# Kernel tuning notes

Measured on AMD Instinct MI355X. Metric: run time of the kernel, lower is better.

## Reference

```python
import jax, jax.numpy as jnp
import numpy as np

B, T, S, D = 8, 512, 512, 1024
NUM_HEADS = 16
REUSE_HEADS = 8
NEW_HEADS = NUM_HEADS - REUSE_HEADS
KEY_DIM = 64
VALUE_DIM = 64
PE_MAX = 512  # pe_max_seq_length


def setup_inputs() -> dict:
    key = jax.random.key(0)
    ks = jax.random.split(key, 12)
    s = 0.02
    return {
        "query": jax.random.normal(ks[0], (B, T, D), jnp.float32),
        "value": jax.random.normal(ks[1], (B, S, D), jnp.float32),
        # scores reused from a previous layer (already softmaxed there)
        "reuse_attention_scores": jax.random.uniform(ks[2], (B, REUSE_HEADS, T, S), jnp.float32),
        "Wq": jax.random.normal(ks[3], (D, NEW_HEADS, KEY_DIM), jnp.float32) * s,
        "bq": jnp.zeros((NEW_HEADS, KEY_DIM), jnp.float32),
        "Wk": jax.random.normal(ks[4], (D, NEW_HEADS, KEY_DIM), jnp.float32) * s,
        "bk": jnp.zeros((NEW_HEADS, KEY_DIM), jnp.float32),
        "Wv": jax.random.normal(ks[5], (D, NUM_HEADS, VALUE_DIM), jnp.float32) * s,
        "bv": jnp.zeros((NUM_HEADS, VALUE_DIM), jnp.float32),
        # relative position embeddings: [1, new_heads, 2*PE_MAX - 1]
        "pos_emb": jax.random.truncated_normal(ks[6], -2.0, 2.0, (1, NEW_HEADS, 2 * PE_MAX - 1), jnp.float32) * 0.2,
        # output denses: one for reused heads (no bias), one for new heads (bias)
        "Wo_reuse": jax.random.normal(ks[7], (REUSE_HEADS, VALUE_DIM, D), jnp.float32) * s,
        "Wo_new": jax.random.normal(ks[8], (NEW_HEADS, VALUE_DIM, D), jnp.float32) * s,
        "bo": jnp.zeros((D,), jnp.float32),
    }


def reference(query, value, reuse_attention_scores, Wq, bq, Wk, bk, Wv, bv,
              pos_emb, Wo_reuse, Wo_new, bo):
    # projections (EinsumDense abc,cde->abde + bias over last two dims)
    q = jnp.einsum("btd,dnh->btnh", query, Wq) + bq           # [B,T,Hn,kd]
    k = jnp.einsum("bsd,dnh->bsnh", value, Wk) + bk           # [B,S,Hn,kd]
    v = jnp.einsum("bsd,dnh->bsnh", value, Wv) + bv           # [B,S,H,vd]
    v_reuse, v_new = v[:, :, :REUSE_HEADS, :], v[:, :, REUSE_HEADS:, :]

    # new-head scores: scaled QK^T  (dot_product_equation 'aecd,abcd->acbe')
    q = q * (1.0 / np.sqrt(float(KEY_DIM)))
    new_scores = jnp.einsum("bsnh,btnh->bnts", k, q)          # [B,Hn,T,S]

    # relative position bias: index = clip(key_pos - query_pos + PE_MAX-1)
    rel = jnp.arange(S)[None, :] - jnp.arange(T)[:, None] + (PE_MAX - 1)
    rel = jnp.clip(rel, 0, 2 * PE_MAX - 2)                    # [T,S]
    bias = pos_emb[0][:, rel]                                 # [Hn,T,S]
    new_scores = jax.nn.softmax(new_scores + bias[None], axis=-1)

    # reused heads consume previous-layer scores directly (dropout=0)
    reuse_scores = reuse_attention_scores[:, :REUSE_HEADS]
    out_reuse = jnp.einsum("bnts,bsnh->btnh", reuse_scores, v_reuse)
    out_new = jnp.einsum("bnts,bsnh->btnh", new_scores, v_new)

    # separate output projections, summed; bias only on the new-heads dense
    out = (jnp.einsum("btnh,nhd->btd", out_reuse, Wo_reuse)
           + jnp.einsum("btnh,nhd->btd", out_new, Wo_new) + bo)
    return out
```

## Files before the change

kernel.cpp:

```cpp
#include <hip/hip_runtime.h>
#include <hip/hip_bf16.h>

typedef __bf16 bf16_t;
typedef __bf16 bf16x8 __attribute__((ext_vector_type(8)));
typedef __bf16 bf16x4v __attribute__((ext_vector_type(4)));
typedef float  f32x4  __attribute__((ext_vector_type(4)));

#define GLDS(gsrc, ldst)                                                              \
  __builtin_amdgcn_global_load_lds(                                                   \
      (const __attribute__((address_space(1))) unsigned int*)(gsrc),                  \
      (__attribute__((address_space(3))) unsigned int*)(ldst), 16, 0, 0)

struct TArgs {
  const float* src[5];
  bf16_t* dst[5];
  int C[5], Ct[5], off[5], blk0[6];
  float scale[5];
};
struct CTArgs {
  const float* qa; bf16_t* qd;
  const float* va; bf16_t* vd;
  TArgs ta;
};
__global__ void k_convtrans(CTArgs ca) {
  __shared__ float tile[32][33];
  const int bid = blockIdx.x;
  if (bid < 4096) {
    int i = bid * 256 + threadIdx.x;
    const float* s; bf16_t* d;
    if (i < 524288) { s = ca.qa; d = ca.qd; } else { s = ca.va; d = ca.vd; i -= 524288; }
    const float4* p = reinterpret_cast<const float4*>(s) + 2 * (long)i;
    float4 x = p[0], y = p[1];
    bf16x8 o;
    o[0] = (bf16_t)x.x; o[1] = (bf16_t)x.y; o[2] = (bf16_t)x.z; o[3] = (bf16_t)x.w;
    o[4] = (bf16_t)y.x; o[5] = (bf16_t)y.y; o[6] = (bf16_t)y.z; o[7] = (bf16_t)y.w;
    reinterpret_cast<bf16x8*>(d)[i] = o;
    return;
  }
  const TArgs& ta = ca.ta;
  const int tb = bid - 4096;
  int s = 0;
  while (tb >= ta.blk0[s + 1]) ++s;
  const int bi = tb - ta.blk0[s];
  const int Ct = ta.Ct[s];
  const int c0 = (bi % Ct) * 32, r0 = (bi / Ct) * 32;
  const int C = ta.C[s];
  const float* src = ta.src[s];
  const int lx = threadIdx.x & 31, ly = threadIdx.x >> 5;
  #pragma unroll
  for (int i = 0; i < 32; i += 8)
    tile[ly + i][lx] = src[(long)(r0 + ly + i) * C + (c0 + lx)];
  __syncthreads();
  const float sc = ta.scale[s];
  bf16_t* dst = ta.dst[s];
  const int off = ta.off[s];
  #pragma unroll
  for (int i = 0; i < 32; i += 8)
    dst[(long)(c0 + ly + i) * 1024 + off + (r0 + lx)] = (bf16_t)(tile[lx][ly + i] * sc);
}

struct ProjItem {
  const bf16_t* A; const bf16_t* B; bf16_t* C; const float* bias;
  float bscale; int ldc; int writeT;
};
struct ProjArgs { ProjItem it[3]; };

__global__ __launch_bounds__(256)
void k_gemm_proj(ProjArgs pa) {
  __shared__ char smem[32768];
  const int bid = blockIdx.x;
  const int z = bid < 128 ? 0 : (bid < 256 ? 1 : 2);
  const int local = bid - (z == 0 ? 0 : (z == 1 ? 128 : 256));
  const ProjItem it = pa.it[z];
  const int t = threadIdx.x, lane = t & 63, wid = t >> 6;
  const int wr = wid >> 1, wc = wid & 1;
  const int m0 = (local & 31) * 128, n0 = (local >> 5) * 128;
  const int lhi = lane >> 4, llo = lane & 15;

  const bf16_t* Ab = it.A + (long)m0 * 1024;
  const bf16_t* Bb = it.B + (long)n0 * 1024;

  const int e0 = t * 8,        r0s = e0 >> 5, c0s = e0 & 31;
  const int e1 = (256 + t) * 8, r1s = e1 >> 5, c1s = e1 & 31;

#define PSTAGE(k0_, bsel)                                                     \
  { bf16_t* bA = (bf16_t*)(smem + (bsel) * 16384);                            \
    bf16_t* bB = (bf16_t*)(smem + (bsel) * 16384 + 8192);                     \
    GLDS(Ab + (long)r0s * 1024 + (k0_) + c0s, bA + wid * 512);                \
    GLDS(Ab + (long)r1s * 1024 + (k0_) + c1s, bA + 2048 + wid * 512);         \
    GLDS(Bb + (long)r0s * 1024 + (k0_) + c0s, bB + wid * 512);                \
    GLDS(Bb + (long)r1s * 1024 + (k0_) + c1s, bB + 2048 + wid * 512); }

  f32x4 acc[4][4] = {};
  PSTAGE(0, 0);
  __syncthreads();
  int cur = 0;
  for (int t32 = 0; t32 < 32; ++t32) {
    bf16_t* sA = (bf16_t*)(smem + cur * 16384);
    bf16_t* sB = (bf16_t*)(smem + cur * 16384 + 8192);
    bf16x8 a[4], b[4];
    #pragma unroll
    for (int mi = 0; mi < 4; ++mi)
      a[mi] = *reinterpret_cast<const bf16x8*>(sA + (wr * 64 + mi * 16 + llo) * 32 + lhi * 8);
    #pragma unroll
    for (int ni = 0; ni < 4; ++ni)
      b[ni] = *reinterpret_cast<const bf16x8*>(sB + (wc * 64 + ni * 16 + llo) * 32 + lhi * 8);
    if (t32 < 31) PSTAGE((t32 + 1) * 32, cur ^ 1);
    #pragma unroll
    for (int mi = 0; mi < 4; ++mi)
      #pragma unroll
      for (int ni = 0; ni < 4; ++ni)
        acc[mi][ni] = __builtin_amdgcn_mfma_f32_16x16x32_bf16(a[mi], b[ni], acc[mi][ni], 0, 0, 0);
    __syncthreads();
    cur ^= 1;
  }
#undef PSTAGE

  #pragma unroll
  for (int mi = 0; mi < 4; ++mi)
    #pragma unroll
    for (int ni = 0; ni < 4; ++ni) {
      const float bv = it.bias[n0 + wc * 64 + ni * 16 + llo] * it.bscale;
      #pragma unroll
      for (int r = 0; r < 4; ++r) acc[mi][ni][r] += bv;
    }

  if (!it.writeT) {
    bf16_t* E = (bf16_t*)smem;
    #pragma unroll
    for (int p = 0; p < 2; ++p) {
      if (wr == p) {
        #pragma unroll
        for (int mi = 0; mi < 4; ++mi)
          #pragma unroll
          for (int ni = 0; ni < 4; ++ni)
            #pragma unroll
            for (int r = 0; r < 4; ++r)
              E[(mi * 16 + lhi * 4 + r) * 136 + wc * 64 + ni * 16 + llo] = (bf16_t)acc[mi][ni][r];
      }
      __syncthreads();
      #pragma unroll
      for (int round = 0; round < 4; ++round) {
        const int row = (t >> 4) + round * 16;
        const int l16 = t & 15;
        float4 v = *reinterpret_cast<const float4*>((char*)E + row * 272 + l16 * 16);
        *reinterpret_cast<float4*>(it.C + (long)(m0 + p * 64 + row) * it.ldc + n0 + l16 * 8) = v;
      }
      __syncthreads();
    }
  } else {
    bf16_t* E = (bf16_t*)smem;
    #pragma unroll
    for (int p = 0; p < 2; ++p) {
      if (wr == p) {
        #pragma unroll
        for (int mi = 0; mi < 4; ++mi)
          #pragma unroll
          for (int ni = 0; ni < 4; ++ni)
            #pragma unroll
            for (int r = 0; r < 4; ++r)
              E[(wc * 64 + ni * 16 + llo) * 72 + mi * 16 + lhi * 4 + r] = (bf16_t)acc[mi][ni][r];
      }
      __syncthreads();
      #pragma unroll
      for (int round = 0; round < 4; ++round) {
        const int nr = (t >> 3) + round * 32;
        const int l8 = t & 7;
        float4 v = *reinterpret_cast<const float4*>((char*)E + nr * 144 + l8 * 16);
        *reinterpret_cast<float4*>(it.C + (long)(n0 + nr) * it.ldc + m0 + p * 64 + l8 * 8) = v;
      }
      __syncthreads();
    }
  }
}

__global__ __launch_bounds__(256)
void k_gemm_out(const bf16_t* __restrict__ A_, const bf16_t* __restrict__ B_,
                float* __restrict__ C_, const float* __restrict__ bias) {
  __shared__ char smem[24576];
  const int t = threadIdx.x, lane = t & 63, wid = t >> 6;
  const int wr = wid >> 1, wc = wid & 1;
  const int m0 = blockIdx.x * 64, n0 = blockIdx.y * 128;
  const int lhi = lane >> 4, llo = lane & 15;

  const bf16_t* Ab = A_ + (long)m0 * 1024;
  const bf16_t* Bb = B_ + (long)n0 * 1024;

  const int e0 = t * 8,        r0s = e0 >> 5, c0s = e0 & 31;
  const int e1 = (256 + t) * 8, r1s = e1 >> 5, c1s = e1 & 31;

#define OSTAGE(k0_, bsel)                                                     \
  { bf16_t* bA = (bf16_t*)(smem + (bsel) * 12288);                            \
    bf16_t* bB = (bf16_t*)(smem + (bsel) * 12288 + 4096);                     \
    GLDS(Ab + (long)r0s * 1024 + (k0_) + c0s, bA + wid * 512);                \
    GLDS(Bb + (long)r0s * 1024 + (k0_) + c0s, bB + wid * 512);                \
    GLDS(Bb + (long)r1s * 1024 + (k0_) + c1s, bB + 2048 + wid * 512); }

  f32x4 acc[2][4] = {};
  OSTAGE(0, 0);
  __syncthreads();
  int cur = 0;
  for (int t32 = 0; t32 < 32; ++t32) {
    bf16_t* sA = (bf16_t*)(smem + cur * 12288);
    bf16_t* sB = (bf16_t*)(smem + cur * 12288 + 4096);
    bf16x8 a[2], b[4];
    #pragma unroll
    for (int mi = 0; mi < 2; ++mi)
      a[mi] = *reinterpret_cast<const bf16x8*>(sA + (wr * 32 + mi * 16 + llo) * 32 + lhi * 8);
    #pragma unroll
    for (int ni = 0; ni < 4; ++ni)
      b[ni] = *reinterpret_cast<const bf16x8*>(sB + (wc * 64 + ni * 16 + llo) * 32 + lhi * 8);
    if (t32 < 31) OSTAGE((t32 + 1) * 32, cur ^ 1);
    #pragma unroll
    for (int mi = 0; mi < 2; ++mi)
      #pragma unroll
      for (int ni = 0; ni < 4; ++ni)
        acc[mi][ni] = __builtin_amdgcn_mfma_f32_16x16x32_bf16(a[mi], b[ni], acc[mi][ni], 0, 0, 0);
    __syncthreads();
    cur ^= 1;
  }
#undef OSTAGE

  #pragma unroll
  for (int mi = 0; mi < 2; ++mi)
    #pragma unroll
    for (int ni = 0; ni < 4; ++ni) {
      const float bv = bias[n0 + wc * 64 + ni * 16 + llo];
      #pragma unroll
      for (int r = 0; r < 4; ++r) acc[mi][ni][r] += bv;
    }

  float* E = (float*)smem;
  #pragma unroll
  for (int p = 0; p < 2; ++p) {
    if (wr == p) {
      #pragma unroll
      for (int mi = 0; mi < 2; ++mi)
        #pragma unroll
        for (int ni = 0; ni < 4; ++ni)
          #pragma unroll
          for (int r = 0; r < 4; ++r)
            E[(mi * 16 + lhi * 4 + r) * 132 + wc * 64 + ni * 16 + llo] = acc[mi][ni][r];
    }
    __syncthreads();
    #pragma unroll
    for (int round = 0; round < 4; ++round) {
      const int row = (t >> 5) + round * 8;
      const int l32 = t & 31;
      float4 v = *reinterpret_cast<const float4*>((char*)E + row * 528 + l32 * 16);
      *reinterpret_cast<float4*>(C_ + (long)(m0 + p * 32 + row) * 1024 + n0 + l32 * 4) = v;
    }
    __syncthreads();
  }
}

__global__ __launch_bounds__(256, 5)
void k_attn_all(const bf16_t* __restrict__ qb, const bf16_t* __restrict__ kb,
                const bf16_t* __restrict__ vbT, const float* __restrict__ pe,
                const float* __restrict__ reuse, bf16_t* __restrict__ om) {
  __shared__ char smem[32768];
  const int bid = blockIdx.x;
  const int r3 = bid % 3;
  const int q3 = bid / 3;
  const int lane = threadIdx.x & 63, w = threadIdx.x >> 6;
  const int lhi = lane >> 4, llo = lane & 15;

  if (r3 == 0) {
    bf16_t* pes2 = (bf16_t*)smem;
    char* KtB = smem + 8192;
    char* VtB = smem + 16384;
    char* PtB = smem + 24576 + w * 2048;

    const int fidx = q3;
    const int tt = fidx >> 6;
    const int bh = fidx & 63;
    const int b = bh >> 3, h = bh & 7;
    const int t0w = tt * 64 + w * 16;

    const bf16_t* Ksrc = kb + (long)(b * 512) * 512 + h * 64;
    const bf16_t* Vsrc = vbT + (long)(512 + h * 64) * 4096 + b * 512;
    const int krow = w * 16 + (lane >> 3);
    const int kcol = ((lane & 7) ^ (lane >> 3)) << 3;
    bf16_t* kdst = (bf16_t*)(KtB + w * 2048);
    bf16_t* vdst = (bf16_t*)(VtB + w * 2048);

#define STAGE_K(it_)                                                                   \
  { _Pragma("unroll")                                                                  \
    for (int g = 0; g < 2; ++g)                                                        \
      GLDS(Ksrc + (long)((it_) * 64 + krow + g * 8) * 512 + kcol, kdst + g * 512); }
#define STAGE_V(it_)                                                                   \
  { _Pragma("unroll")                                                                  \
    for (int g = 0; g < 2; ++g)                                                        \
      GLDS(Vsrc + (long)(krow + g * 8) * 4096 + (it_) * 64 + kcol, vdst + g * 512); }

    STAGE_K(0);
    STAGE_V(0);

    const bf16_t* Qb = qb + (long)(b * 512 + t0w + llo) * 512 + h * 64;
    bf16x8 qf0 = *reinterpret_cast<const bf16x8*>(Qb + lhi * 8);
    bf16x8 qf1 = *reinterpret_cast<const bf16x8*>(Qb + 32 + lhi * 8);
    {
      const float* peh = pe + h * 1023;
      for (int j = threadIdx.x; j < 4092; j += 256) {
        const int d = j >> 2, st = j & 3;
        int idx = d + 16 * st; if (idx > 1022) idx = 1022;
        pes2[j] = (bf16_t)peh[idx];
      }
    }

    f32x4 oacc[4] = {};
    float lr[4] = {0.f, 0.f, 0.f, 0.f};

    __syncthreads();

    for (int it = 0; it < 8; ++it) {
      const int s0 = it * 64;

      f32x4 acc[4] = {};
      #pragma unroll
      for (int st = 0; st < 4; ++st) {
        const int rowb = st * 16 + llo;
        const int sw = (rowb & 7) << 4;
        bf16x8 kf0 = *reinterpret_cast<const bf16x8*>(KtB + rowb * 128 + ((lhi * 16) ^ sw));
        bf16x8 kf1 = *reinterpret_cast<const bf16x8*>(KtB + rowb * 128 + ((64 + lhi * 16) ^ sw));
        acc[st] = __builtin_amdgcn_mfma_f32_16x16x32_bf16(qf0, kf0, acc[st], 0, 0, 0);
        acc[st] = __builtin_amdgcn_mfma_f32_16x16x32_bf16(qf1, kf1, acc[st], 0, 0, 0);
      }

      __syncthreads();
      if (it < 7) STAGE_K(it + 1);

      #pragma unroll
      for (int r = 0; r < 4; ++r) {
        const int tl = lhi * 4 + r;
        const int bidx = s0 + llo - (t0w + tl) + 511;
        const bf16x4v pb = *reinterpret_cast<const bf16x4v*>(pes2 + bidx * 4);
        const int swp = (tl & 7) << 4;
        float lp = 0.f;
        #pragma unroll
        for (int st = 0; st < 4; ++st) {
          const float e = __expf(acc[st][r] + (float)pb[st]);
          lp += e;
          *reinterpret_cast<bf16_t*>(PtB + tl * 128 + (((st * 16 + llo) * 2) ^ swp)) = (bf16_t)e;
        }
        lr[r] += lp;
      }

      const int swa = (llo & 7) << 4;
      #pragma unroll
      for (int ks = 0; ks < 2; ++ks) {
        bf16x8 pav = *reinterpret_cast<const bf16x8*>(PtB + llo * 128 + ((ks * 64 + lhi * 16) ^ swa));
        #pragma unroll
        for (int ni = 0; ni < 4; ++ni) {
          const int rowv = ni * 16 + llo;
          bf16x8 vf = *reinterpret_cast<const bf16x8*>(VtB + rowv * 128 + ((ks * 64 + lhi * 16) ^ ((rowv & 7) << 4)));
          oacc[ni] = __builtin_amdgcn_mfma_f32_16x16x32_bf16(pav, vf, oacc[ni], 0, 0, 0);
        }
      }

      __syncthreads();
      if (it < 7) STAGE_V(it + 1);
    }

    #pragma unroll
    for (int r = 0; r < 4; ++r) {
      lr[r] += __shfl_xor(lr[r], 1);
      lr[r] += __shfl_xor(lr[r], 2);
      lr[r] += __shfl_xor(lr[r], 4);
      lr[r] += __shfl_xor(lr[r], 8);
    }

    bf16_t* Ew = (bf16_t*)(smem + 8192 + w * 4096);
    #pragma unroll
    for (int ni = 0; ni < 4; ++ni)
      #pragma unroll
      for (int r = 0; r < 4; ++r)
        Ew[(lhi * 4 + r) * 72 + ni * 16 + llo] = (bf16_t)(oacc[ni][r] * (1.f / lr[r]));
    #pragma unroll
    for (int round = 0; round < 2; ++round) {
      const int lr8 = (lane >> 3) + round * 8;
      const int l8 = lane & 7;
      float4 v = *reinterpret_cast<const float4*>((char*)Ew + lr8 * 144 + l8 * 16);
      *reinterpret_cast<float4*>(om + (long)(b * 512 + t0w + lr8) * 1024 + 512 + h * 64 + l8 * 8) = v;
    }
#undef STAGE_K
#undef STAGE_V
    return;
  }

  typedef float RedRow[32][68];
  RedRow* red = (RedRow*)smem;
  const int pidx = q3 * 2 + (r3 - 1);
  const int bh = pidx & 63;
  const int mt = pidx >> 6;
  const int b = bh >> 3, head = bh & 7;
  const int m0 = mt * 32;
  const int ks0 = w * 128;

  const float*  Af = reuse + (long)b * 2097152 + (long)head * 262144;
  const bf16_t* Bp = vbT + (long)(head * 64) * 4096 + b * 512;

  f32x4 acc[2][4] = {};
  float4 Ax[2][2][2];
  bf16x8 Bx[2][4];

  #define PV_LOAD(kq, buf)                                                              \
    {                                                                                   \
      const int kk = ks0 + (kq) * 32 + lhi * 8;                                         \
      _Pragma("unroll")                                                                 \
      for (int mi = 0; mi < 2; ++mi) {                                                  \
        const float4* p = reinterpret_cast<const float4*>(Af + (long)(m0 + mi * 16 + llo) * 512 + kk); \
        Ax[buf][mi][0] = p[0];                                                          \
        Ax[buf][mi][1] = p[1];                                                          \
      }                                                                                 \
      _Pragma("unroll")                                                                 \
      for (int ni = 0; ni < 4; ++ni)                                                    \
        Bx[buf][ni] = *reinterpret_cast<const bf16x8*>(Bp + (long)(ni * 16 + llo) * 4096 + kk); \
    }

  PV_LOAD(0, 0);
  #pragma unroll
  for (int kq = 0; kq < 4; ++kq) {
    const int cb = kq & 1;
    if (kq < 3) {
      const int nb = (kq + 1) & 1;
      PV_LOAD(kq + 1, nb);
    }
    bf16x8 a[2];
    #pragma unroll
    for (int mi = 0; mi < 2; ++mi) {
      float4 x = Ax[cb][mi][0], y = Ax[cb][mi][1];
      bf16x8 tv;
      tv[0] = (bf16_t)x.x; tv[1] = (bf16_t)x.y; tv[2] = (bf16_t)x.z; tv[3] = (bf16_t)x.w;
      tv[4] = (bf16_t)y.x; tv[5] = (bf16_t)y.y; tv[6] = (bf16_t)y.z; tv[7] = (bf16_t)y.w;
      a[mi] = tv;
    }
    #pragma unroll
    for (int mi = 0; mi < 2; ++mi)
      #pragma unroll
      for (int ni = 0; ni < 4; ++ni)
        acc[mi][ni] = __builtin_amdgcn_mfma_f32_16x16x32_bf16(a[mi], Bx[cb][ni], acc[mi][ni], 0, 0, 0);
  }
  #undef PV_LOAD

  if (w >= 2) {
    #pragma unroll
    for (int mi = 0; mi < 2; ++mi)
      #pragma unroll
      for (int ni = 0; ni < 4; ++ni)
        #pragma unroll
        for (int r = 0; r < 4; ++r)
          red[w - 2][mi * 16 + lhi * 4 + r][ni * 16 + llo] = acc[mi][ni][r];
  }
  __syncthreads();
  if (w < 2) {
    #pragma unroll
    for (int mi = 0; mi < 2; ++mi)
      #pragma unroll
      for (int ni = 0; ni < 4; ++ni)
        #pragma unroll
        for (int r = 0; r < 4; ++r)
          acc[mi][ni][r] += red[w][mi * 16 + lhi * 4 + r][ni * 16 + llo];
  }
  __syncthreads();
  if (w == 1) {
    #pragma unroll
    for (int mi = 0; mi < 2; ++mi)
      #pragma unroll
      for (int ni = 0; ni < 4; ++ni)
        #pragma unroll
        for (int r = 0; r < 4; ++r)
          red[0][mi * 16 + lhi * 4 + r][ni * 16 + llo] = acc[mi][ni][r];
  }
  __syncthreads();
  if (w == 0) {
    bf16_t* E = (bf16_t*)&red[1][0][0];
    #pragma unroll
    for (int mi = 0; mi < 2; ++mi)
      #pragma unroll
      for (int ni = 0; ni < 4; ++ni)
        #pragma unroll
        for (int r = 0; r < 4; ++r) {
          const int mr = mi * 16 + lhi * 4 + r;
          const int nn = ni * 16 + llo;
          E[mr * 72 + nn] = (bf16_t)(acc[mi][ni][r] + red[0][mr][nn]);
        }
    bf16_t* Cb = om + (long)b * 524288 + head * 64;
    #pragma unroll
    for (int round = 0; round < 4; ++round) {
      const int row = (lane >> 3) + round * 8;
      const int l8 = lane & 7;
      float4 v = *reinterpret_cast<const float4*>((char*)E + row * 144 + l8 * 16);
      *reinterpret_cast<float4*>(Cb + (long)(m0 + row) * 1024 + l8 * 8) = v;
    }
  }
}

extern "C" void kernel_launch(void* const* d_in, const int* in_sizes, int n_in,
                              void* d_out, int out_size, void* d_ws, size_t ws_size,
                              hipStream_t stream) {
  const float* query = (const float*)d_in[0];
  const float* value = (const float*)d_in[1];
  const float* reuse = (const float*)d_in[2];
  const float* Wq    = (const float*)d_in[3];
  const float* bq    = (const float*)d_in[4];
  const float* Wk    = (const float*)d_in[5];
  const float* bk    = (const float*)d_in[6];
  const float* Wv    = (const float*)d_in[7];
  const float* bv    = (const float*)d_in[8];
  const float* pe    = (const float*)d_in[9];
  const float* WoR   = (const float*)d_in[10];
  const float* WoN   = (const float*)d_in[11];
  const float* bo    = (const float*)d_in[12];
  float* out = (float*)d_out;
  (void)in_sizes; (void)n_in; (void)out_size; (void)ws_size;

  char* w = (char*)d_ws;
  bf16_t* qx  = (bf16_t*)(w);
  bf16_t* vx  = (bf16_t*)(w + (8L  << 20));
  bf16_t* WqT = (bf16_t*)(w + (16L << 20));
  bf16_t* WkT = (bf16_t*)(w + (17L << 20));
  bf16_t* WvT = (bf16_t*)(w + (18L << 20));
  bf16_t* WoT = (bf16_t*)(w + (20L << 20));
  bf16_t* qb  = (bf16_t*)(w + (22L << 20));
  bf16_t* kb  = (bf16_t*)(w + (26L << 20));
  bf16_t* vbT = (bf16_t*)(w + (30L << 20));
  bf16_t* om  = (bf16_t*)(w + (38L << 20));

  CTArgs ca;
  ca.qa = query; ca.qd = qx; ca.va = value; ca.vd = vx;
  ca.ta.src[0] = Wq;  ca.ta.dst[0] = WqT; ca.ta.C[0] = 512;  ca.ta.Ct[0] = 16; ca.ta.off[0] = 0;   ca.ta.scale[0] = 0.125f;
  ca.ta.src[1] = Wk;  ca.ta.dst[1] = WkT; ca.ta.C[1] = 512;  ca.ta.Ct[1] = 16; ca.ta.off[1] = 0;   ca.ta.scale[1] = 1.f;
  ca.ta.src[2] = Wv;  ca.ta.dst[2] = WvT; ca.ta.C[2] = 1024; ca.ta.Ct[2] = 32; ca.ta.off[2] = 0;   ca.ta.scale[2] = 1.f;
  ca.ta.src[3] = WoR; ca.ta.dst[3] = WoT; ca.ta.C[3] = 1024; ca.ta.Ct[3] = 32; ca.ta.off[3] = 0;   ca.ta.scale[3] = 1.f;
  ca.ta.src[4] = WoN; ca.ta.dst[4] = WoT; ca.ta.C[4] = 1024; ca.ta.Ct[4] = 32; ca.ta.off[4] = 512; ca.ta.scale[4] = 1.f;
  ca.ta.blk0[0] = 0; ca.ta.blk0[1] = 512; ca.ta.blk0[2] = 1024; ca.ta.blk0[3] = 2048; ca.ta.blk0[4] = 2560; ca.ta.blk0[5] = 3072;
  k_convtrans<<<dim3(7168), 256, 0, stream>>>(ca);

  ProjArgs pa;
  pa.it[0] = { qx, WqT, qb,  bq, 0.125f, 512,  0 };
  pa.it[1] = { vx, WkT, kb,  bk, 1.f,    512,  0 };
  pa.it[2] = { vx, WvT, vbT, bv, 1.f,    4096, 1 };
  k_gemm_proj<<<dim3(512), 256, 0, stream>>>(pa);

  k_attn_all<<<dim3(1536), 256, 0, stream>>>(qb, kb, vbT, pe, reuse, om);

  k_gemm_out<<<dim3(64, 8), 256, 0, stream>>>(om, WoT, out, bo);
}
```

Before: 90.06 us.

## Restructure reuse-head PV blocks to per-warp row tiles without split-K reduction

After: 104.7 us. +16.2%, slower.

```diff
diff --git a/kernel.cpp b/kernel.cpp
--- a/kernel.cpp
+++ b/kernel.cpp
@@ -254,24 +254,22 @@
   }
 }
 
-__global__ __launch_bounds__(256, 5)
+__global__ __launch_bounds__(256, 4)
 void k_attn_all(const bf16_t* __restrict__ qb, const bf16_t* __restrict__ kb,
                 const bf16_t* __restrict__ vbT, const float* __restrict__ pe,
                 const float* __restrict__ reuse, bf16_t* __restrict__ om) {
   __shared__ char smem[32768];
   const int bid = blockIdx.x;
-  const int r3 = bid % 3;
-  const int q3 = bid / 3;
   const int lane = threadIdx.x & 63, w = threadIdx.x >> 6;
   const int lhi = lane >> 4, llo = lane & 15;
 
-  if (r3 == 0) {
+  if ((bid & 1) == 0) {
     bf16_t* pes2 = (bf16_t*)smem;
     char* KtB = smem + 8192;
     char* VtB = smem + 16384;
     char* PtB = smem + 24576 + w * 2048;
 
-    const int fidx = q3;
+    const int fidx = bid >> 1;
     const int tt = fidx >> 6;
     const int bh = fidx & 63;
     const int b = bh >> 3, h = bh & 7;
@@ -388,111 +386,63 @@
     return;
   }
 
-  typedef float RedRow[32][68];
-  RedRow* red = (RedRow*)smem;
-  const int pidx = q3 * 2 + (r3 - 1);
+  const int pidx = bid >> 1;
+  const int mt = pidx >> 6;
   const int bh = pidx & 63;
-  const int mt = pidx >> 6;
   const int b = bh >> 3, head = bh & 7;
-  const int m0 = mt * 32;
-  const int ks0 = w * 128;
-
-  const float*  Af = reuse + (long)b * 2097152 + (long)head * 262144;
+  const int m0 = mt * 64 + w * 16;
+
+  const float* Af = reuse + (long)b * 2097152 + (long)head * 262144 + (long)(m0 + llo) * 512;
   const bf16_t* Bp = vbT + (long)(head * 64) * 4096 + b * 512;
 
-  f32x4 acc[2][4] = {};
-  float4 Ax[2][2][2];
-  bf16x8 Bx[2][4];
-
-  #define PV_LOAD(kq, buf)                                                              \
-    {                                                                                   \
-      const int kk = ks0 + (kq) * 32 + lhi * 8;                                         \
-      _Pragma("unroll")                                                                 \
-      for (int mi = 0; mi < 2; ++mi) {                                                  \
-        const float4* p = reinterpret_cast<const float4*>(Af + (long)(m0 + mi * 16 + llo) * 512 + kk); \
-        Ax[buf][mi][0] = p[0];                                                          \
-        Ax[buf][mi][1] = p[1];                                                          \
-      }                                                                                 \
-      _Pragma("unroll")                                                                 \
+  f32x4 acc[4] = {};
+  float4 Ax[3][2];
+  bf16x8 Bx[3][4];
+
+  #define A_LOAD(kq, buf)                                                               \
+    { const float4* p = reinterpret_cast<const float4*>(Af + (kq) * 32 + lhi * 8);      \
+      Ax[buf][0] = p[0];                                                                \
+      Ax[buf][1] = p[1]; }
+  #define B_LOAD(kq, buf)                                                               \
+    { _Pragma("unroll")                                                                 \
       for (int ni = 0; ni < 4; ++ni)                                                    \
-        Bx[buf][ni] = *reinterpret_cast<const bf16x8*>(Bp + (long)(ni * 16 + llo) * 4096 + kk); \
-    }
-
-  PV_LOAD(0, 0);
-  #pragma unroll
-  for (int kq = 0; kq < 4; ++kq) {
-    const int cb = kq & 1;
-    if (kq < 3) {
-      const int nb = (kq + 1) & 1;
-      PV_LOAD(kq + 1, nb);
-    }
-    bf16x8 a[2];
-    #pragma unroll
-    for (int mi = 0; mi < 2; ++mi) {
-      float4 x = Ax[cb][mi][0], y = Ax[cb][mi][1];
-      bf16x8 tv;
-      tv[0] = (bf16_t)x.x; tv[1] = (bf16_t)x.y; tv[2] = (bf16_t)x.z; tv[3] = (bf16_t)x.w;
-      tv[4] = (bf16_t)y.x; tv[5] = (bf16_t)y.y; tv[6] = (bf16_t)y.z; tv[7] = (bf16_t)y.w;
-      a[mi] = tv;
-    }
-    #pragma unroll
-    for (int mi = 0; mi < 2; ++mi)
-      #pragma unroll
-      for (int ni = 0; ni < 4; ++ni)
-        acc[mi][ni] = __builtin_amdgcn_mfma_f32_16x16x32_bf16(a[mi], Bx[cb][ni], acc[mi][ni], 0, 0, 0);
-  }
-  #undef PV_LOAD
-
-  if (w >= 2) {
-    #pragma unroll
-    for (int mi = 0; mi < 2; ++mi)
-      #pragma unroll
-      for (int ni = 0; ni < 4; ++ni)
-        #pragma unroll
-        for (int r = 0; r < 4; ++r)
-          red[w - 2][mi * 16 + lhi * 4 + r][ni * 16 + llo] = acc[mi][ni][r];
-  }
-  __syncthreads();
-  if (w < 2) {
-    #pragma unroll
-    for (int mi = 0; mi < 2; ++mi)
-      #pragma unroll
-      for (int ni = 0; ni < 4; ++ni)
-        #pragma unroll
-        for (int r = 0; r < 4; ++r)
-          acc[mi][ni][r] += red[w][mi * 16 + lhi * 4 + r][ni * 16 + llo];
-  }
-  __syncthreads();
-  if (w == 1) {
-    #pragma unroll
-    for (int mi = 0; mi < 2; ++mi)
-      #pragma unroll
-      for (int ni = 0; ni < 4; ++ni)
-        #pragma unroll
-        for (int r = 0; r < 4; ++r)
-          red[0][mi * 16 + lhi * 4 + r][ni * 16 + llo] = acc[mi][ni][r];
-  }
-  __syncthreads();
-  if (w == 0) {
-    bf16_t* E = (bf16_t*)&red[1][0][0];
-    #pragma unroll
-    for (int mi = 0; mi < 2; ++mi)
-      #pragma unroll
-      for (int ni = 0; ni < 4; ++ni)
-        #pragma unroll
-        for (int r = 0; r < 4; ++r) {
-          const int mr = mi * 16 + lhi * 4 + r;
-          const int nn = ni * 16 + llo;
-          E[mr * 72 + nn] = (bf16_t)(acc[mi][ni][r] + red[0][mr][nn]);
-        }
-    bf16_t* Cb = om + (long)b * 524288 + head * 64;
-    #pragma unroll
-    for (int round = 0; round < 4; ++round) {
-      const int row = (lane >> 3) + round * 8;
-      const int l8 = lane & 7;
-      float4 v = *reinterpret_cast<const float4*>((char*)E + row * 144 + l8 * 16);
-      *reinterpret_cast<float4*>(Cb + (long)(m0 + row) * 1024 + l8 * 8) = v;
-    }
+        Bx[buf][ni] = *reinterpret_cast<const bf16x8*>(Bp + (long)(ni * 16 + llo) * 4096 + (kq) * 32 + lhi * 8); }
+
+  A_LOAD(0, 0); B_LOAD(0, 0);
+  A_LOAD(1, 1); B_LOAD(1, 1);
+  #pragma unroll
+  for (int kq = 0; kq < 16; ++kq) {
+    const int cu_ = kq % 3;
+    if (kq < 14) {
+      const int nb = (kq + 2) % 3;
+      A_LOAD(kq + 2, nb);
+      B_LOAD(kq + 2, nb);
+    }
+    bf16x8 av;
+    {
+      const float4 x = Ax[cu_][0], y = Ax[cu_][1];
+      av[0] = (bf16_t)x.x; av[1] = (bf16_t)x.y; av[2] = (bf16_t)x.z; av[3] = (bf16_t)x.w;
+      av[4] = (bf16_t)y.x; av[5] = (bf16_t)y.y; av[6] = (bf16_t)y.z; av[7] = (bf16_t)y.w;
+    }
+    #pragma unroll
+    for (int ni = 0; ni < 4; ++ni)
+      acc[ni] = __builtin_amdgcn_mfma_f32_16x16x32_bf16(av, Bx[cu_][ni], acc[ni], 0, 0, 0);
+  }
+  #undef A_LOAD
+  #undef B_LOAD
+
+  bf16_t* Ew = (bf16_t*)(smem + w * 2304);
+  #pragma unroll
+  for (int ni = 0; ni < 4; ++ni)
+    #pragma unroll
+    for (int r = 0; r < 4; ++r)
+      Ew[(lhi * 4 + r) * 72 + ni * 16 + llo] = (bf16_t)acc[ni][r];
+  #pragma unroll
+  for (int round = 0; round < 2; ++round) {
+    const int row = (lane >> 3) + round * 8;
+    const int l8 = lane & 7;
+    float4 v = *reinterpret_cast<const float4*>((char*)Ew + row * 144 + l8 * 16);
+    *reinterpret_cast<float4*>(om + (long)b * 524288 + (long)(m0 + row) * 1024 + head * 64 + l8 * 8) = v;
   }
 }
 
@@ -543,7 +493,7 @@
   pa.it[2] = { vx, WvT, vbT, bv, 1.f,    4096, 1 };
   k_gemm_proj<<<dim3(512), 256, 0, stream>>>(pa);
 
-  k_attn_all<<<dim3(1536), 256, 0, stream>>>(qb, kb, vbT, pe, reuse, om);
+  k_attn_all<<<dim3(1024), 256, 0, stream>>>(qb, kb, vbT, pe, reuse, om);
 
   k_gemm_out<<<dim3(64, 8), 256, 0, stream>>>(om, WoT, out, bo);
 }
```
